# Kernel optimization log

Measured on AMD Instinct MI355X. Metric: run time of the kernel, lower is better.

## Reference

```python
import jax, jax.numpy as jnp
import numpy as np

N0, N1, N2 = 10000, 40000, 160000
E1, E2 = 240000, 960000
C_IN, C_MID, C_OUT = 64, 32, 16  # up_convs = [64, 32, 16]


def _basis(pseudo):
    """Open quadratic B-spline basis, kernel_size=3, degree=2, dim=2.
    With kernel_size-degree == 1, v = pseudo in [0,1) and all 3 basis fns per dim
    are active with fixed indices 0..2, so the 2-D product gives 9 weights/edge."""
    t = pseudo  # [E, 2]
    b = jnp.stack([0.5 * (1.0 - t) ** 2, -t * t + t + 0.5, 0.5 * t * t], axis=-1)  # [E,2,3]
    return (b[:, 0, :, None] * b[:, 1, None, :]).reshape(t.shape[0], 9)  # [E, 9]


def _spline_conv(x, src, dst, basis, W, R, b, n):
    # x: [N, Cin], W: [9, Cin, Cout], R: [Cin, Cout], b: [Cout]
    xs = x[src]  # [E, Cin] gather
    m = basis[:, 0:1] * (xs @ W[0])
    for k in range(1, 9):  # fixed small kernel loop; avoids [E,9,Cout] blowup
        m = m + basis[:, k:k + 1] * (xs @ W[k])
    agg = jax.ops.segment_sum(m, dst, num_segments=n)  # aggr='add'
    return agg + x @ R + b


def _up_level(x_coarse, unpool, edge, pseudo, skip, W1, R1, b1, W2, R2, b2):
    n = unpool.shape[0]
    x = x_coarse[unpool]          # MeshUnpool: copy coarse features to fine verts
    basis = _basis(pseudo)
    src, dst = edge[0], edge[1]
    h = jax.nn.relu(_spline_conv(x, src, dst, basis, W1, R1, b1, n))
    h = jnp.concatenate([h, skip], axis=1)  # [n, 2*Cout] == Cin
    h = jax.nn.relu(_spline_conv(h, src, dst, basis, W1, R1, b1, n))  # conv1 reused
    h = jax.nn.relu(_spline_conv(h, src, dst, basis, W2, R2, b2, n))
    return h


def setup_inputs() -> dict:
    key = jax.random.key(0)
    ks = jax.random.split(key, 24)
    s = 0.05
    inp = {
        'x0': jax.random.normal(ks[0], (N0, C_IN), jnp.float32),
        'unpool1': jax.random.randint(ks[1], (N1,), 0, N0),
        'edge1': jax.random.randint(ks[2], (2, E1), 0, N1),
        'pseudo1': jax.random.uniform(ks[3], (E1, 2), jnp.float32),
        'skip1': jax.random.normal(ks[4], (N1, C_MID), jnp.float32),
        'unpool2': jax.random.randint(ks[5], (N2,), 0, N1),
        'edge2': jax.random.randint(ks[6], (2, E2), 0, N2),
        'pseudo2': jax.random.uniform(ks[7], (E2, 2), jnp.float32),
        'skip2': jax.random.normal(ks[8], (N2, C_OUT), jnp.float32),
        # level 1 (UpConv 64 -> 32)
        'W1a': jax.random.normal(ks[9], (9, C_IN, C_MID), jnp.float32) * s,
        'R1a': jax.random.normal(ks[10], (C_IN, C_MID), jnp.float32) * s,
        'b1a': jax.random.normal(ks[11], (C_MID,), jnp.float32) * s,
        'W2a': jax.random.normal(ks[12], (9, C_MID, C_MID), jnp.float32) * s,
        'R2a': jax.random.normal(ks[13], (C_MID, C_MID), jnp.float32) * s,
        'b2a': jax.random.normal(ks[14], (C_MID,), jnp.float32) * s,
        # level 2 (UpConv 32 -> 16)
        'W1b': jax.random.normal(ks[15], (9, C_MID, C_OUT), jnp.float32) * s,
        'R1b': jax.random.normal(ks[16], (C_MID, C_OUT), jnp.float32) * s,
        'b1b': jax.random.normal(ks[17], (C_OUT,), jnp.float32) * s,
        'W2b': jax.random.normal(ks[18], (9, C_OUT, C_OUT), jnp.float32) * s,
        'R2b': jax.random.normal(ks[19], (C_OUT, C_OUT), jnp.float32) * s,
        'b2b': jax.random.normal(ks[20], (C_OUT,), jnp.float32) * s,
    }
    return inp


def reference(x0, unpool1, edge1, pseudo1, skip1, unpool2, edge2, pseudo2, skip2,
              W1a, R1a, b1a, W2a, R2a, b2a, W1b, R1b, b1b, W2b, R2b, b2b):
    h1 = _up_level(x0, unpool1, edge1, pseudo1, skip1, W1a, R1a, b1a, W2a, R2a, b2a)
    h2 = _up_level(h1, unpool2, edge2, pseudo2, skip2, W1b, R1b, b1b, W2b, R2b, b2b)
    return h2
```

## Files before the change

### kernel.cpp

```cpp
#include <hip/hip_runtime.h>
#include <stdint.h>

typedef __bf16 bf16x8 __attribute__((ext_vector_type(8)));
typedef __bf16 bf16x4 __attribute__((ext_vector_type(4)));
typedef float  f32x4  __attribute__((ext_vector_type(4)));

__device__ __forceinline__ void d_pack(int o,
    const float* W1a, const float* R1a, const float* W2a, const float* R2a,
    const float* W1b, const float* R1b, const float* W2b, const float* R2b,
    __bf16* BpA, __bf16* BpB, __bf16* BpC, __bf16* BpD) {
  const float *W, *R; __bf16* Bp; int Cin, Cout;
  if (o < 20480)      { W = W1a; R = R1a; Bp = BpA; Cin = 64; Cout = 32; }
  else if (o < 30720) { W = W2a; R = R2a; Bp = BpB; Cin = 32; Cout = 32; o -= 20480; }
  else if (o < 35840) { W = W1b; R = R1b; Bp = BpC; Cin = 32; Cout = 16; o -= 30720; }
  else if (o < 38400) { W = W2b; R = R2b; Bp = BpD; Cin = 16; Cout = 16; o -= 35840; }
  else return;
  int CT = Cout / 16;
  int j = o & 7, lane = (o >> 3) & 63, tile = o >> 9;
  int ct = tile % CT, kc = tile / CT;
  int k = kc * 32 + ((lane >> 4) * 8) + j;
  int n = ct * 16 + (lane & 15);
  float v;
  if (k < 9 * Cin) { int k9 = k / Cin, cin = k - k9 * Cin; v = W[(k9 * Cin + cin) * Cout + n]; }
  else             { v = R[(k - 9 * Cin) * Cout + n]; }
  Bp[o] = (__bf16)v;
}

__device__ __forceinline__ void d_bhist(int b, int t, const int* dst, int E,
                                        int* bcnt, int nbk) {
  __shared__ int h[256];
  h[t] = 0;
  __syncthreads();
  int e0 = b * 2048 + t * 8;
  if (e0 + 8 <= E) {
    int4 a = *reinterpret_cast<const int4*>(dst + e0);
    int4 c = *reinterpret_cast<const int4*>(dst + e0 + 4);
    atomicAdd(&h[a.x >> 10], 1); atomicAdd(&h[a.y >> 10], 1);
    atomicAdd(&h[a.z >> 10], 1); atomicAdd(&h[a.w >> 10], 1);
    atomicAdd(&h[c.x >> 10], 1); atomicAdd(&h[c.y >> 10], 1);
    atomicAdd(&h[c.z >> 10], 1); atomicAdd(&h[c.w >> 10], 1);
  } else {
    for (int j = 0; j < 8; ++j)
      if (e0 + j < E) atomicAdd(&h[dst[e0 + j] >> 10], 1);
  }
  __syncthreads();
  if (t < nbk && h[t]) atomicAdd(&bcnt[t], h[t]);
}

__global__ __launch_bounds__(256) void k_prologue(
    const float* __restrict__ W1a, const float* __restrict__ R1a,
    const float* __restrict__ W2a, const float* __restrict__ R2a,
    const float* __restrict__ W1b, const float* __restrict__ R1b,
    const float* __restrict__ W2b, const float* __restrict__ R2b,
    __bf16* __restrict__ BpA, __bf16* __restrict__ BpB,
    __bf16* __restrict__ BpC, __bf16* __restrict__ BpD,
    const float4* __restrict__ x0, __bf16* __restrict__ x0bf,
    const int* __restrict__ dst1, int E1, int* __restrict__ bcnt1, int nbk1,
    const int* __restrict__ dst2, int E2, int* __restrict__ bcnt2, int nbk2) {
  int b = blockIdx.x, t = threadIdx.x;
  if (b < 150) {
    d_pack(b * 256 + t, W1a, R1a, W2a, R2a, W1b, R1b, W2b, R2b, BpA, BpB, BpC, BpD);
  } else if (b < 775) {
    int i = (b - 150) * 256 + t;
    if (i < 160000) {
      float4 v = x0[i];
      bf16x4 o = {(__bf16)v.x, (__bf16)v.y, (__bf16)v.z, (__bf16)v.w};
      *reinterpret_cast<bf16x4*>(x0bf + (size_t)i * 4) = o;
    }
  } else if (b < 893) {
    d_bhist(b - 775, t, dst1, E1, bcnt1, nbk1);
  } else {
    d_bhist(b - 893, t, dst2, E2, bcnt2, nbk2);
  }
}

__global__ void k_bscan_dual(const int* __restrict__ bcnt1, int nbk1, int E1,
                             int* __restrict__ bstart1, int* __restrict__ bcur1,
                             const int* __restrict__ bcnt2, int nbk2, int E2,
                             int* __restrict__ bstart2, int* __restrict__ bcur2) {
  const int* bcnt; int nbk, E; int *bstart, *bcur;
  if (blockIdx.x == 0) { bcnt = bcnt1; nbk = nbk1; E = E1; bstart = bstart1; bcur = bcur1; }
  else                 { bcnt = bcnt2; nbk = nbk2; E = E2; bstart = bstart2; bcur = bcur2; }
  __shared__ int wsum[4];
  int t = threadIdx.x, lane = t & 63, w = t >> 6;
  int v = (t < nbk) ? bcnt[t] : 0;
  int x = v;
  #pragma unroll
  for (int o = 1; o < 64; o <<= 1) { int y = __shfl_up(x, o, 64); if (lane >= o) x += y; }
  if (lane == 63) wsum[w] = x;
  __syncthreads();
  int wpre = 0;
  #pragma unroll
  for (int k = 0; k < 4; ++k) if (k < w) wpre += wsum[k];
  int excl = wpre + x - v;
  if (t < nbk) { bstart[t] = excl; bcur[t] = excl; }
  if (t == 0) bstart[nbk] = E;
}

__device__ __forceinline__ void d_bpart(int b, int t, const int* src, const int* dst,
                                        const float2* pse, const int* up, int E, int* bcur,
                                        uint2* ebuf, uint16_t* rbuf, int nbk) {
  __shared__ int h[256];
  __shared__ int base[256];
  h[t] = 0;
  __syncthreads();
  int e0 = b * 2048 + t * 8;
  int d[8], rank[8];
  bool full = (e0 + 8 <= E);
  if (full) {
    int4 a = *reinterpret_cast<const int4*>(dst + e0);
    int4 c = *reinterpret_cast<const int4*>(dst + e0 + 4);
    d[0] = a.x; d[1] = a.y; d[2] = a.z; d[3] = a.w;
    d[4] = c.x; d[5] = c.y; d[6] = c.z; d[7] = c.w;
    #pragma unroll
    for (int j = 0; j < 8; ++j) rank[j] = atomicAdd(&h[d[j] >> 10], 1);
  } else {
    #pragma unroll
    for (int j = 0; j < 8; ++j)
      if (e0 + j < E) { d[j] = dst[e0 + j]; rank[j] = atomicAdd(&h[d[j] >> 10], 1); }
  }
  __syncthreads();
  if (t < nbk && h[t]) base[t] = atomicAdd(&bcur[t], h[t]);
  __syncthreads();
  if (full) {
    int4 a = *reinterpret_cast<const int4*>(src + e0);
    int4 c = *reinterpret_cast<const int4*>(src + e0 + 4);
    int s[8] = {a.x, a.y, a.z, a.w, c.x, c.y, c.z, c.w};
    int u[8];
    #pragma unroll
    for (int j = 0; j < 8; ++j) u[j] = up[s[j]];
    float2 p[8];
    #pragma unroll
    for (int j = 0; j < 8; ++j) p[j] = pse[e0 + j];
    #pragma unroll
    for (int j = 0; j < 8; ++j) {
      int bkt = d[j] >> 10, dloc = d[j] & 1023;
      union { uint uu; _Float16 hh[2]; } cv;
      cv.hh[0] = (_Float16)p[j].x; cv.hh[1] = (_Float16)p[j].y;
      int pos = base[bkt] + rank[j];
      ebuf[pos] = make_uint2((uint)s[j] | ((uint)dloc << 18), cv.uu);
      rbuf[pos] = (uint16_t)u[j];
    }
  } else {
    #pragma unroll
    for (int j = 0; j < 8; ++j) {
      if (e0 + j >= E) continue;
      int bkt = d[j] >> 10, dloc = d[j] & 1023;
      int sj = src[e0 + j];
      float2 p = pse[e0 + j];
      union { uint uu; _Float16 hh[2]; } cv;
      cv.hh[0] = (_Float16)p.x; cv.hh[1] = (_Float16)p.y;
      int pos = base[bkt] + rank[j];
      ebuf[pos] = make_uint2((uint)sj | ((uint)dloc << 18), cv.uu);
      rbuf[pos] = (uint16_t)up[sj];
    }
  }
}

__global__ __launch_bounds__(256) void k_bpart_dual(
    const int* __restrict__ src1, const int* __restrict__ dst1, const float2* __restrict__ pse1,
    const int* __restrict__ up1, int E1, int* __restrict__ bcur1,
    uint2* __restrict__ ebuf1, uint16_t* __restrict__ rbuf1, int nbk1, int NB1,
    const int* __restrict__ src2, const int* __restrict__ dst2, const float2* __restrict__ pse2,
    const int* __restrict__ up2, int E2, int* __restrict__ bcur2,
    uint2* __restrict__ ebuf2, uint16_t* __restrict__ rbuf2, int nbk2) {
  int b = blockIdx.x, t = threadIdx.x;
  if (b < NB1) d_bpart(b, t, src1, dst1, pse1, up1, E1, bcur1, ebuf1, rbuf1, nbk1);
  else         d_bpart(b - NB1, t, src2, dst2, pse2, up2, E2, bcur2, ebuf2, rbuf2, nbk2);
}

__device__ __forceinline__ void d_bcsr(int b, int t, const int* bstart, const uint2* ebuf,
                                       const uint16_t* rbuf, uint2* epk, uint2* epkR,
                                       int* off, int N, int E, int nbk) {
  __shared__ int cnt[1024];
  __shared__ int excl[1024];
  __shared__ int cur[1024];
  __shared__ int wsum[4];
  int e0 = bstart[b], e1 = bstart[b + 1];
  #pragma unroll
  for (int k = 0; k < 4; ++k) { cnt[t * 4 + k] = 0; cur[t * 4 + k] = 0; }
  __syncthreads();
  for (int i = e0 + t; i < e1; i += 256)
    atomicAdd(&cnt[(ebuf[i].x >> 18) & 1023], 1);
  __syncthreads();
  int lane = t & 63, w = t >> 6;
  int i0 = t * 4;
  int c0 = cnt[i0], c1 = cnt[i0 + 1], c2 = cnt[i0 + 2], c3 = cnt[i0 + 3];
  int s = c0 + c1 + c2 + c3, x = s;
  #pragma unroll
  for (int o = 1; o < 64; o <<= 1) { int y = __shfl_up(x, o, 64); if (lane >= o) x += y; }
  if (lane == 63) wsum[w] = x;
  __syncthreads();
  int wpre = 0;
  #pragma unroll
  for (int k = 0; k < 4; ++k) if (k < w) wpre += wsum[k];
  int ex = wpre + x - s;
  excl[i0] = ex; excl[i0 + 1] = ex + c0; excl[i0 + 2] = ex + c0 + c1; excl[i0 + 3] = ex + c0 + c1 + c2;
  int dg0 = b * 1024;
  int exv[4] = {ex, ex + c0, ex + c0 + c1, ex + c0 + c1 + c2};
  #pragma unroll
  for (int k = 0; k < 4; ++k) {
    int d = dg0 + i0 + k;
    if (d < N) off[d] = e0 + exv[k];
  }
  __syncthreads();
  for (int i = e0 + t; i < e1; i += 256) {
    uint2 r = ebuf[i];
    uint rs = rbuf[i];
    int dloc = (r.x >> 18) & 1023;
    int rk = atomicAdd(&cur[dloc], 1);
    int pos = e0 + excl[dloc] + rk;
    epk[pos]  = make_uint2(r.x & 0x3FFFFu, r.y);
    epkR[pos] = make_uint2(rs, r.y);
  }
  if (b == nbk - 1 && t == 0) off[N] = E;
}

__global__ __launch_bounds__(256) void k_bcsr_dual(
    const int* __restrict__ bstart1, const uint2* __restrict__ ebuf1,
    const uint16_t* __restrict__ rbuf1, uint2* __restrict__ epk1, uint2* __restrict__ epkR1,
    int* __restrict__ off1, int N1, int E1, int nbk1,
    const int* __restrict__ bstart2, const uint2* __restrict__ ebuf2,
    const uint16_t* __restrict__ rbuf2, uint2* __restrict__ epk2, uint2* __restrict__ epkR2,
    int* __restrict__ off2, int N2, int E2, int nbk2) {
  int b = blockIdx.x, t = threadIdx.x;
  if (b < nbk1) d_bcsr(b, t, bstart1, ebuf1, rbuf1, epk1, epkR1, off1, N1, E1, nbk1);
  else          d_bcsr(b - nbk1, t, bstart2, ebuf2, rbuf2, epk2, epkR2, off2, N2, E2, nbk2);
}

__device__ __forceinline__ void edge1(uint ps, const bf16x4 xf, float (&acc)[9][4]) {
  union { uint u; _Float16 h[2]; } cv; cv.u = ps;
  float t0 = (float)cv.h[0], t1 = (float)cv.h[1];
  float u0 = 1.f - t0;
  float wi[3] = {0.5f * u0 * u0, -t0 * t0 + t0 + 0.5f, 0.5f * t0 * t0};
  float u1 = 1.f - t1;
  float wj[3] = {0.5f * u1 * u1, -t1 * t1 + t1 + 0.5f, 0.5f * t1 * t1};
  float xfv[4];
  #pragma unroll
  for (int v = 0; v < 4; ++v) xfv[v] = (float)xf[v];
  #pragma unroll
  for (int ki = 0; ki < 3; ++ki)
    #pragma unroll
    for (int kj = 0; kj < 3; ++kj) {
      float w = wi[ki] * wj[kj];
      #pragma unroll
      for (int v = 0; v < 4; ++v)
        acc[ki * 3 + kj][v] += w * xfv[v];
    }
}

template<int Cin, int Cout, bool OUTF32, bool HAS_SKIP, bool REMAP>
__global__ __launch_bounds__(256, 4) void k_conv(
                        const int* __restrict__ off,
                        const uint2* __restrict__ epk,
                        const __bf16* __restrict__ X, const __bf16* __restrict__ Bp,
                        const float* __restrict__ bias, const float* __restrict__ skip,
                        const int* __restrict__ up,
                        void* __restrict__ outv, int N, int outStride) {
  constexpr int LPD = Cin / 4;
  constexpr int DPB = 256 / LPD;
  constexpr int K   = 10 * Cin;
  constexpr int KP2 = K + 8;
  constexpr int NT  = DPB / 16;
  constexpr int KC  = K / 32;
  constexpr int CT  = Cout / 16;
  constexpr int UNITS = NT * CT;

  __shared__ __bf16 As[DPB * KP2];

  int t = threadIdx.x;
  int g = t / LPD, sub = t % LPD;
  int d = blockIdx.x * DPB + g;

  float acc[9][4];
  #pragma unroll
  for (int k = 0; k < 9; ++k)
    #pragma unroll
    for (int v = 0; v < 4; ++v) acc[k][v] = 0.f;
  bf16x4 xd = {};

  if (d < N) {
    int dsrc = d;
    if constexpr (REMAP) dsrc = up[d];
    xd = *reinterpret_cast<const bf16x4*>(X + (size_t)dsrc * Cin + sub * 4);
    const __bf16* Xs = X + sub * 4;
    int b0 = off[d], b1 = off[d + 1];
    int i = b0;
    for (; i + 8 <= b1; i += 8) {
      uint2 e0 = epk[i],     e1 = epk[i + 1], e2 = epk[i + 2], e3 = epk[i + 3];
      uint2 e4 = epk[i + 4], e5 = epk[i + 5], e6 = epk[i + 6], e7 = epk[i + 7];
      bf16x4 x0v = *reinterpret_cast<const bf16x4*>(Xs + (size_t)e0.x * Cin);
      bf16x4 x1v = *reinterpret_cast<const bf16x4*>(Xs + (size_t)e1.x * Cin);
      bf16x4 x2v = *reinterpret_cast<const bf16x4*>(Xs + (size_t)e2.x * Cin);
      bf16x4 x3v = *reinterpret_cast<const bf16x4*>(Xs + (size_t)e3.x * Cin);
      bf16x4 x4v = *reinterpret_cast<const bf16x4*>(Xs + (size_t)e4.x * Cin);
      bf16x4 x5v = *reinterpret_cast<const bf16x4*>(Xs + (size_t)e5.x * Cin);
      bf16x4 x6v = *reinterpret_cast<const bf16x4*>(Xs + (size_t)e6.x * Cin);
      bf16x4 x7v = *reinterpret_cast<const bf16x4*>(Xs + (size_t)e7.x * Cin);
      edge1(e0.y, x0v, acc); edge1(e1.y, x1v, acc);
      edge1(e2.y, x2v, acc); edge1(e3.y, x3v, acc);
      edge1(e4.y, x4v, acc); edge1(e5.y, x5v, acc);
      edge1(e6.y, x6v, acc); edge1(e7.y, x7v, acc);
    }
    for (; i + 4 <= b1; i += 4) {
      uint2 e0 = epk[i], e1 = epk[i + 1], e2 = epk[i + 2], e3 = epk[i + 3];
      bf16x4 x0v = *reinterpret_cast<const bf16x4*>(Xs + (size_t)e0.x * Cin);
      bf16x4 x1v = *reinterpret_cast<const bf16x4*>(Xs + (size_t)e1.x * Cin);
      bf16x4 x2v = *reinterpret_cast<const bf16x4*>(Xs + (size_t)e2.x * Cin);
      bf16x4 x3v = *reinterpret_cast<const bf16x4*>(Xs + (size_t)e3.x * Cin);
      edge1(e0.y, x0v, acc); edge1(e1.y, x1v, acc);
      edge1(e2.y, x2v, acc); edge1(e3.y, x3v, acc);
    }
    for (; i < b1; ++i) {
      uint2 ep = epk[i];
      bf16x4 xf = *reinterpret_cast<const bf16x4*>(Xs + (size_t)ep.x * Cin);
      edge1(ep.y, xf, acc);
    }
  }

  __bf16* row = As + (size_t)g * KP2;
  #pragma unroll
  for (int k = 0; k < 9; ++k) {
    bf16x4 tmp;
    #pragma unroll
    for (int v = 0; v < 4; ++v) tmp[v] = (__bf16)acc[k][v];
    *reinterpret_cast<bf16x4*>(row + k * Cin + sub * 4) = tmp;
  }
  *reinterpret_cast<bf16x4*>(row + 9 * Cin + sub * 4) = xd;
  __syncthreads();

  int lane = t & 63, wave = t >> 6;
  int c15 = lane & 15, q = lane >> 4;
  for (int u = wave; u < UNITS; u += 4) {
    int tile = u / CT, ct = u - tile * CT;
    const __bf16* arow = As + (size_t)(tile * 16 + c15) * KP2 + q * 8;
    f32x4 a4 = {0.f, 0.f, 0.f, 0.f};
    #pragma unroll
    for (int kc = 0; kc < KC; ++kc) {
      bf16x8 a = *reinterpret_cast<const bf16x8*>(arow + kc * 32);
      bf16x8 b = *reinterpret_cast<const bf16x8*>(Bp + ((size_t)(kc * CT + ct) * 64 + lane) * 8);
      a4 = __builtin_amdgcn_mfma_f32_16x16x32_bf16(a, b, a4, 0, 0, 0);
    }
    int cout = ct * 16 + c15;
    float bb = bias[cout];
    #pragma unroll
    for (int r = 0; r < 4; ++r) {
      int m = q * 4 + r;
      int dd = blockIdx.x * DPB + tile * 16 + m;
      if (dd < N) {
        float vv = fmaxf(a4[r] + bb, 0.f);
        if constexpr (OUTF32)
          ((float*)outv)[(size_t)dd * outStride + cout] = vv;
        else
          ((__bf16*)outv)[(size_t)dd * outStride + cout] = (__bf16)vv;
        if constexpr (HAS_SKIP) {
          float sv = skip[(size_t)dd * Cout + cout];
          ((__bf16*)outv)[(size_t)dd * outStride + Cout + cout] = (__bf16)sv;
        }
      }
    }
  }
}

extern "C" void kernel_launch(void* const* d_in, const int* in_sizes, int n_in,
                              void* d_out, int out_size, void* d_ws, size_t ws_size,
                              hipStream_t stream) {
  const float* x0      = (const float*)d_in[0];
  const int*   up1     = (const int*)d_in[1];
  const int*   edge1v  = (const int*)d_in[2];
  const float* pseudo1 = (const float*)d_in[3];
  const float* skip1   = (const float*)d_in[4];
  const int*   up2     = (const int*)d_in[5];
  const int*   edge2v  = (const int*)d_in[6];
  const float* pseudo2 = (const float*)d_in[7];
  const float* skip2   = (const float*)d_in[8];
  const float* W1a = (const float*)d_in[9];
  const float* R1a = (const float*)d_in[10];
  const float* b1a = (const float*)d_in[11];
  const float* W2a = (const float*)d_in[12];
  const float* R2a = (const float*)d_in[13];
  const float* b2a = (const float*)d_in[14];
  const float* W1b = (const float*)d_in[15];
  const float* R1b = (const float*)d_in[16];
  const float* b1b = (const float*)d_in[17];
  const float* W2b = (const float*)d_in[18];
  const float* R2b = (const float*)d_in[19];
  const float* b2b = (const float*)d_in[20];

  const int N1 = 40000, N2 = 160000, E1 = 240000, E2 = 960000;
  const int NBK1 = 40, NBK2 = 157;
  const int NB1 = (E1 + 2047) / 2048;
  const int NB2 = (E2 + 2047) / 2048;

  char* ws = (char*)d_ws;
  __bf16* x0bf   = (__bf16*)(ws);
  __bf16* xcat1  = (__bf16*)(ws +  1280000);
  __bf16* x3     = (__bf16*)(ws +  6400000);
  __bf16* h1     = (__bf16*)(ws +  8960000);
  __bf16* xcat2  = (__bf16*)(ws + 11520000);
  __bf16* x6     = (__bf16*)(ws + 21760000);
  int*   off1    = (int*)(ws + 26880000);
  int*   off2    = (int*)(ws + 27040016);
  uint2* ebuf1   = (uint2*)(ws + 27680032);
  uint2* epk1    = (uint2*)(ws + 29600032);
  uint2* epkR1   = (uint2*)(ws + 31520032);
  uint16_t* rbuf1 = (uint16_t*)(ws + 33440032);
  uint2* ebuf2   = (uint2*)(ws + 33920032);
  uint2* epk2    = (uint2*)(ws + 41600032);
  uint2* epkR2   = (uint2*)(ws + 49280032);
  uint16_t* rbuf2 = (uint16_t*)(ws + 56960032);
  int*   bcnt12  = (int*)(ws + 58880032);
  int*   bstart1 = (int*)(ws + 58882080);
  int*   bcur1   = (int*)(ws + 58882336);
  int*   bstart2 = (int*)(ws + 58882592);
  int*   bcur2   = (int*)(ws + 58883616);
  __bf16* BpA    = (__bf16*)(ws + 58884640);
  __bf16* BpB    = (__bf16*)(ws + 58925600);
  __bf16* BpC    = (__bf16*)(ws + 58946080);
  __bf16* BpD    = (__bf16*)(ws + 58956320);
  int* bcnt1 = bcnt12, *bcnt2 = bcnt12 + 256;

  hipMemsetAsync(bcnt12, 0, 512 * 4, stream);

  k_prologue<<<150 + 625 + NB1 + NB2, 256, 0, stream>>>(
      W1a, R1a, W2a, R2a, W1b, R1b, W2b, R2b, BpA, BpB, BpC, BpD,
      (const float4*)x0, x0bf,
      edge1v + E1, E1, bcnt1, NBK1,
      edge2v + E2, E2, bcnt2, NBK2);

  k_bscan_dual<<<2, 256, 0, stream>>>(bcnt1, NBK1, E1, bstart1, bcur1,
                                      bcnt2, NBK2, E2, bstart2, bcur2);

  k_bpart_dual<<<NB1 + NB2, 256, 0, stream>>>(
      edge1v, edge1v + E1, (const float2*)pseudo1, up1, E1, bcur1, ebuf1, rbuf1, NBK1, NB1,
      edge2v, edge2v + E2, (const float2*)pseudo2, up2, E2, bcur2, ebuf2, rbuf2, NBK2);

  k_bcsr_dual<<<NBK1 + NBK2, 256, 0, stream>>>(
      bstart1, ebuf1, rbuf1, epk1, epkR1, off1, N1, E1, NBK1,
      bstart2, ebuf2, rbuf2, epk2, epkR2, off2, N2, E2, NBK2);

  k_conv<64, 32, false, true,  true ><<<N1 / 16, 256, 0, stream>>>(off1, epkR1, x0bf, BpA, b1a, skip1, up1, xcat1, N1, 64);
  k_conv<64, 32, false, false, false><<<N1 / 16, 256, 0, stream>>>(off1, epk1, xcat1, BpA, b1a, nullptr, nullptr, x3, N1, 32);
  k_conv<32, 32, false, false, false><<<N1 / 32, 256, 0, stream>>>(off1, epk1, x3, BpB, b2a, nullptr, nullptr, h1, N1, 32);

  k_conv<32, 16, false, true,  true ><<<N2 / 32, 256, 0, stream>>>(off2, epkR2, h1, BpC, b1b, skip2, up2, xcat2, N2, 32);
  k_conv<32, 16, false, false, false><<<N2 / 32, 256, 0, stream>>>(off2, epk2, xcat2, BpC, b1b, nullptr, nullptr, x6, N2, 16);
  k_conv<16, 16, true,  false, false><<<N2 / 64, 256, 0, stream>>>(off2, epk2, x6, BpD, b2b, nullptr, nullptr, d_out, N2, 16);
}
```

Before: 351.6 us.

## Sort destination nodes by in-degree to balance per-lane edge loops

Builds a degree histogram during CSR construction, prefix-sums it in descending order, and scatters node ids into a degree-sorted permutation. Each conv kernel then processes destinations through this permutation, so threads in a wavefront have similar edge counts and less divergence. Output rows are written through the permutation via shared memory. It also drops the 8-wide unrolled edge loop and raises the occupancy hint for Cin<=32 kernels. The cost is two extra small launches and scattered, non-contiguous output writes and self-feature reads.

```diff
diff --git a/kernel.cpp b/kernel.cpp
--- a/kernel.cpp
+++ b/kernel.cpp
@@ -171,14 +171,16 @@
 
 __device__ __forceinline__ void d_bcsr(int b, int t, const int* bstart, const uint2* ebuf,
                                        const uint16_t* rbuf, uint2* epk, uint2* epkR,
-                                       int* off, int N, int E, int nbk) {
+                                       int* off, int* dhist, int N, int E, int nbk) {
   __shared__ int cnt[1024];
   __shared__ int excl[1024];
   __shared__ int cur[1024];
   __shared__ int wsum[4];
+  __shared__ int lh[64];
   int e0 = bstart[b], e1 = bstart[b + 1];
   #pragma unroll
   for (int k = 0; k < 4; ++k) { cnt[t * 4 + k] = 0; cur[t * 4 + k] = 0; }
+  if (t < 64) lh[t] = 0;
   __syncthreads();
   for (int i = e0 + t; i < e1; i += 256)
     atomicAdd(&cnt[(ebuf[i].x >> 18) & 1023], 1);
@@ -198,10 +200,15 @@
   excl[i0] = ex; excl[i0 + 1] = ex + c0; excl[i0 + 2] = ex + c0 + c1; excl[i0 + 3] = ex + c0 + c1 + c2;
   int dg0 = b * 1024;
   int exv[4] = {ex, ex + c0, ex + c0 + c1, ex + c0 + c1 + c2};
+  int cv4[4] = {c0, c1, c2, c3};
   #pragma unroll
   for (int k = 0; k < 4; ++k) {
     int d = dg0 + i0 + k;
-    if (d < N) off[d] = e0 + exv[k];
+    if (d < N) {
+      off[d] = e0 + exv[k];
+      int c = cv4[k] > 63 ? 63 : cv4[k];
+      atomicAdd(&lh[c], 1);
+    }
   }
   __syncthreads();
   for (int i = e0 + t; i < e1; i += 256) {
@@ -213,19 +220,52 @@
     epk[pos]  = make_uint2(r.x & 0x3FFFFu, r.y);
     epkR[pos] = make_uint2(rs, r.y);
   }
+  if (t < 64 && lh[t]) atomicAdd(&dhist[t], lh[t]);
   if (b == nbk - 1 && t == 0) off[N] = E;
 }
 
 __global__ __launch_bounds__(256) void k_bcsr_dual(
     const int* __restrict__ bstart1, const uint2* __restrict__ ebuf1,
     const uint16_t* __restrict__ rbuf1, uint2* __restrict__ epk1, uint2* __restrict__ epkR1,
-    int* __restrict__ off1, int N1, int E1, int nbk1,
+    int* __restrict__ off1, int* __restrict__ dh1, int N1, int E1, int nbk1,
     const int* __restrict__ bstart2, const uint2* __restrict__ ebuf2,
     const uint16_t* __restrict__ rbuf2, uint2* __restrict__ epk2, uint2* __restrict__ epkR2,
-    int* __restrict__ off2, int N2, int E2, int nbk2) {
+    int* __restrict__ off2, int* __restrict__ dh2, int N2, int E2, int nbk2) {
   int b = blockIdx.x, t = threadIdx.x;
-  if (b < nbk1) d_bcsr(b, t, bstart1, ebuf1, rbuf1, epk1, epkR1, off1, N1, E1, nbk1);
-  else          d_bcsr(b - nbk1, t, bstart2, ebuf2, rbuf2, epk2, epkR2, off2, N2, E2, nbk2);
+  if (b < nbk1) d_bcsr(b, t, bstart1, ebuf1, rbuf1, epk1, epkR1, off1, dh1, N1, E1, nbk1);
+  else          d_bcsr(b - nbk1, t, bstart2, ebuf2, rbuf2, epk2, epkR2, off2, dh2, N2, E2, nbk2);
+}
+
+__global__ void k_dprep(int* __restrict__ dh1, int* __restrict__ dh2) {
+  int* dh = (blockIdx.x == 0) ? dh1 : dh2;
+  if (threadIdx.x == 0) {
+    int run = 0;
+    for (int b = 63; b >= 0; --b) { int c = dh[b]; dh[b] = run; run += c; }
+  }
+}
+
+__global__ __launch_bounds__(256) void k_dscatter(
+    const int* __restrict__ off1, int N1, int* __restrict__ dh1, int* __restrict__ dperm1,
+    const int* __restrict__ off2, int N2, int* __restrict__ dh2, int* __restrict__ dperm2,
+    int NB1s) {
+  __shared__ int lh[64], lbase[64];
+  int b = blockIdx.x, t = threadIdx.x;
+  const int* off; int N; int* dh; int* dperm; int i;
+  if (b < NB1s) { off = off1; N = N1; dh = dh1; dperm = dperm1; i = b * 256 + t; }
+  else          { off = off2; N = N2; dh = dh2; dperm = dperm2; i = (b - NB1s) * 256 + t; }
+  if (t < 64) lh[t] = 0;
+  __syncthreads();
+  int bin = 0, rank = 0;
+  bool valid = (i < N);
+  if (valid) {
+    int deg = off[i + 1] - off[i];
+    bin = deg > 63 ? 63 : deg;
+    rank = atomicAdd(&lh[bin], 1);
+  }
+  __syncthreads();
+  if (t < 64 && lh[t]) lbase[t] = atomicAdd(&dh[t], lh[t]);
+  __syncthreads();
+  if (valid) dperm[lbase[bin] + rank] = i;
 }
 
 __device__ __forceinline__ void edge1(uint ps, const bf16x4 xf, float (&acc)[9][4]) {
@@ -250,9 +290,10 @@
 }
 
 template<int Cin, int Cout, bool OUTF32, bool HAS_SKIP, bool REMAP>
-__global__ __launch_bounds__(256, 4) void k_conv(
+__global__ __launch_bounds__(256, (Cin <= 32 ? 8 : 4)) void k_conv(
                         const int* __restrict__ off,
                         const uint2* __restrict__ epk,
+                        const int* __restrict__ dperm,
                         const __bf16* __restrict__ X, const __bf16* __restrict__ Bp,
                         const float* __restrict__ bias, const float* __restrict__ skip,
                         const int* __restrict__ up,
@@ -267,10 +308,12 @@
   constexpr int UNITS = NT * CT;
 
   __shared__ __bf16 As[DPB * KP2];
+  __shared__ int dpe[DPB];
 
   int t = threadIdx.x;
   int g = t / LPD, sub = t % LPD;
-  int d = blockIdx.x * DPB + g;
+  if (t < DPB) dpe[t] = dperm[blockIdx.x * DPB + t];
+  int d = dperm[blockIdx.x * DPB + g];
 
   float acc[9][4];
   #pragma unroll
@@ -279,29 +322,13 @@
     for (int v = 0; v < 4; ++v) acc[k][v] = 0.f;
   bf16x4 xd = {};
 
-  if (d < N) {
+  {
     int dsrc = d;
     if constexpr (REMAP) dsrc = up[d];
     xd = *reinterpret_cast<const bf16x4*>(X + (size_t)dsrc * Cin + sub * 4);
     const __bf16* Xs = X + sub * 4;
     int b0 = off[d], b1 = off[d + 1];
     int i = b0;
-    for (; i + 8 <= b1; i += 8) {
-      uint2 e0 = epk[i],     e1 = epk[i + 1], e2 = epk[i + 2], e3 = epk[i + 3];
-      uint2 e4 = epk[i + 4], e5 = epk[i + 5], e6 = epk[i + 6], e7 = epk[i + 7];
-      bf16x4 x0v = *reinterpret_cast<const bf16x4*>(Xs + (size_t)e0.x * Cin);
-      bf16x4 x1v = *reinterpret_cast<const bf16x4*>(Xs + (size_t)e1.x * Cin);
-      bf16x4 x2v = *reinterpret_cast<const bf16x4*>(Xs + (size_t)e2.x * Cin);
-      bf16x4 x3v = *reinterpret_cast<const bf16x4*>(Xs + (size_t)e3.x * Cin);
-      bf16x4 x4v = *reinterpret_cast<const bf16x4*>(Xs + (size_t)e4.x * Cin);
-      bf16x4 x5v = *reinterpret_cast<const bf16x4*>(Xs + (size_t)e5.x * Cin);
-      bf16x4 x6v = *reinterpret_cast<const bf16x4*>(Xs + (size_t)e6.x * Cin);
-      bf16x4 x7v = *reinterpret_cast<const bf16x4*>(Xs + (size_t)e7.x * Cin);
-      edge1(e0.y, x0v, acc); edge1(e1.y, x1v, acc);
-      edge1(e2.y, x2v, acc); edge1(e3.y, x3v, acc);
-      edge1(e4.y, x4v, acc); edge1(e5.y, x5v, acc);
-      edge1(e6.y, x6v, acc); edge1(e7.y, x7v, acc);
-    }
     for (; i + 4 <= b1; i += 4) {
       uint2 e0 = epk[i], e1 = epk[i + 1], e2 = epk[i + 2], e3 = epk[i + 3];
       bf16x4 x0v = *reinterpret_cast<const bf16x4*>(Xs + (size_t)e0.x * Cin);
@@ -346,17 +373,15 @@
     #pragma unroll
     for (int r = 0; r < 4; ++r) {
       int m = q * 4 + r;
-      int dd = blockIdx.x * DPB + tile * 16 + m;
-      if (dd < N) {
-        float vv = fmaxf(a4[r] + bb, 0.f);
-        if constexpr (OUTF32)
-          ((float*)outv)[(size_t)dd * outStride + cout] = vv;
-        else
-          ((__bf16*)outv)[(size_t)dd * outStride + cout] = (__bf16)vv;
-        if constexpr (HAS_SKIP) {
-          float sv = skip[(size_t)dd * Cout + cout];
-          ((__bf16*)outv)[(size_t)dd * outStride + Cout + cout] = (__bf16)sv;
-        }
+      int dd = dpe[tile * 16 + m];
+      float vv = fmaxf(a4[r] + bb, 0.f);
+      if constexpr (OUTF32)
+        ((float*)outv)[(size_t)dd * outStride + cout] = vv;
+      else
+        ((__bf16*)outv)[(size_t)dd * outStride + cout] = (__bf16)vv;
+      if constexpr (HAS_SKIP) {
+        float sv = skip[(size_t)dd * Cout + cout];
+        ((__bf16*)outv)[(size_t)dd * outStride + Cout + cout] = (__bf16)sv;
       }
     }
   }
@@ -391,6 +416,8 @@
   const int NBK1 = 40, NBK2 = 157;
   const int NB1 = (E1 + 2047) / 2048;
   const int NB2 = (E2 + 2047) / 2048;
+  const int NB1s = (N1 + 255) / 256;
+  const int NB2s = (N2 + 255) / 256;
 
   char* ws = (char*)d_ws;
   __bf16* x0bf   = (__bf16*)(ws);
@@ -410,17 +437,21 @@
   uint2* epkR2   = (uint2*)(ws + 49280032);
   uint16_t* rbuf2 = (uint16_t*)(ws + 56960032);
   int*   bcnt12  = (int*)(ws + 58880032);
-  int*   bstart1 = (int*)(ws + 58882080);
-  int*   bcur1   = (int*)(ws + 58882336);
-  int*   bstart2 = (int*)(ws + 58882592);
-  int*   bcur2   = (int*)(ws + 58883616);
-  __bf16* BpA    = (__bf16*)(ws + 58884640);
-  __bf16* BpB    = (__bf16*)(ws + 58925600);
-  __bf16* BpC    = (__bf16*)(ws + 58946080);
-  __bf16* BpD    = (__bf16*)(ws + 58956320);
+  int*   dh1     = (int*)(ws + 58882080);
+  int*   dh2     = (int*)(ws + 58882336);
+  int*   bstart1 = (int*)(ws + 58882592);
+  int*   bcur1   = (int*)(ws + 58882848);
+  int*   bstart2 = (int*)(ws + 58883104);
+  int*   bcur2   = (int*)(ws + 58884128);
+  __bf16* BpA    = (__bf16*)(ws + 58885152);
+  __bf16* BpB    = (__bf16*)(ws + 58926112);
+  __bf16* BpC    = (__bf16*)(ws + 58946592);
+  __bf16* BpD    = (__bf16*)(ws + 58956832);
+  int*   dperm1  = (int*)(ws + 58961952);
+  int*   dperm2  = (int*)(ws + 59121952);
   int* bcnt1 = bcnt12, *bcnt2 = bcnt12 + 256;
 
-  hipMemsetAsync(bcnt12, 0, 512 * 4, stream);
+  hipMemsetAsync(bcnt12, 0, 2048 + 512, stream);
 
   k_prologue<<<150 + 625 + NB1 + NB2, 256, 0, stream>>>(
       W1a, R1a, W2a, R2a, W1b, R1b, W2b, R2b, BpA, BpB, BpC, BpD,
@@ -436,14 +467,19 @@
       edge2v, edge2v + E2, (const float2*)pseudo2, up2, E2, bcur2, ebuf2, rbuf2, NBK2);
 
   k_bcsr_dual<<<NBK1 + NBK2, 256, 0, stream>>>(
-      bstart1, ebuf1, rbuf1, epk1, epkR1, off1, N1, E1, NBK1,
-      bstart2, ebuf2, rbuf2, epk2, epkR2, off2, N2, E2, NBK2);
-
-  k_conv<64, 32, false, true,  true ><<<N1 / 16, 256, 0, stream>>>(off1, epkR1, x0bf, BpA, b1a, skip1, up1, xcat1, N1, 64);
-  k_conv<64, 32, false, false, false><<<N1 / 16, 256, 0, stream>>>(off1, epk1, xcat1, BpA, b1a, nullptr, nullptr, x3, N1, 32);
-  k_conv<32, 32, false, false, false><<<N1 / 32, 256, 0, stream>>>(off1, epk1, x3, BpB, b2a, nullptr, nullptr, h1, N1, 32);
-
-  k_conv<32, 16, false, true,  true ><<<N2 / 32, 256, 0, stream>>>(off2, epkR2, h1, BpC, b1b, skip2, up2, xcat2, N2, 32);
-  k_conv<32, 16, false, false, false><<<N2 / 32, 256, 0, stream>>>(off2, epk2, xcat2, BpC, b1b, nullptr, nullptr, x6, N2, 16);
-  k_conv<16, 16, true,  false, false><<<N2 / 64, 256, 0, stream>>>(off2, epk2, x6, BpD, b2b, nullptr, nullptr, d_out, N2, 16);
-}
+      bstart1, ebuf1, rbuf1, epk1, epkR1, off1, dh1, N1, E1, NBK1,
+      bstart2, ebuf2, rbuf2, epk2, epkR2, off2, dh2, N2, E2, NBK2);
+
+  k_dprep<<<2, 64, 0, stream>>>(dh1, dh2);
+
+  k_dscatter<<<NB1s + NB2s, 256, 0, stream>>>(off1, N1, dh1, dperm1,
+                                              off2, N2, dh2, dperm2, NB1s);
+
+  k_conv<64, 32, false, true,  true ><<<N1 / 16, 256, 0, stream>>>(off1, epkR1, dperm1, x0bf, BpA, b1a, skip1, up1, xcat1, N1, 64);
+  k_conv<64, 32, false, false, false><<<N1 / 16, 256, 0, stream>>>(off1, epk1, dperm1, xcat1, BpA, b1a, nullptr, nullptr, x3, N1, 32);
+  k_conv<32, 32, false, false, false><<<N1 / 32, 256, 0, stream>>>(off1, epk1, dperm1, x3, BpB, b2a, nullptr, nullptr, h1, N1, 32);
+
+  k_conv<32, 16, false, true,  true ><<<N2 / 32, 256, 0, stream>>>(off2, epkR2, dperm2, h1, BpC, b1b, skip2, up2, xcat2, N2, 32);
+  k_conv<32, 16, false, false, false><<<N2 / 32, 256, 0, stream>>>(off2, epk2, dperm2, xcat2, BpC, b1b, nullptr, nullptr, x6, N2, 16);
+  k_conv<16, 16, true,  false, false><<<N2 / 64, 256, 0, stream>>>(off2, epk2, dperm2, x6, BpD, b2b, nullptr, nullptr, d_out, N2, 16);
+}
```

Result: faster. 312.2 us (-11.2%).
